# Kernel tuning notes

Measured on AMD Instinct MI355X. Metric: run time of the kernel, lower is better.

## Reference

```python
import jax, jax.numpy as jnp
import numpy as np

B, T, C, H = 4, 2048, 768, 12
D = C // H  # head dim = 64

def setup_inputs() -> dict:
    key = jax.random.key(0)
    k1, k2, k3 = jax.random.split(key, 3)
    x = jax.random.normal(k1, (B, T, C), dtype=jnp.float32)
    W_attn = jax.random.normal(k2, (C, 3 * C), dtype=jnp.float32) * 0.02
    b_attn = jnp.zeros((3 * C,), dtype=jnp.float32)
    W_proj = jax.random.normal(k3, (C, C), dtype=jnp.float32) * 0.02
    b_proj = jnp.zeros((C,), dtype=jnp.float32)
    return {"x": x, "W_attn": W_attn, "b_attn": b_attn, "W_proj": W_proj, "b_proj": b_proj}

def reference(x, W_attn, b_attn, W_proj, b_proj):
    Bx, Tx, Cx = x.shape
    qkv = x @ W_attn + b_attn                      # [B,T,3C]
    q, k, v = jnp.split(qkv, 3, axis=2)
    q = q.reshape(Bx, Tx, H, D).swapaxes(1, 2)     # [B,H,T,D]
    k = k.reshape(Bx, Tx, H, D).swapaxes(1, 2)
    v = v.reshape(Bx, Tx, H, D).swapaxes(1, 2)
    att = jnp.einsum('bhqd,bhkd->bhqk', q, k) / jnp.sqrt(jnp.float32(D))
    mask = jnp.tril(jnp.ones((Tx, Tx), dtype=bool))
    att = jnp.where(mask, att, -jnp.inf)
    att = jax.nn.softmax(att, axis=-1)
    y = jnp.einsum('bhqk,bhkd->bhqd', att, v)      # [B,H,T,D]
    y = y.swapaxes(1, 2).reshape(Bx, Tx, Cx)
    return y @ W_proj + b_proj
```

## Files before the change

kernel.cpp:

```cpp
#include <hip/hip_runtime.h>
#include <hip/hip_bf16.h>

#define BATCH 4
#define TSEQ  2048
#define CDIM  768
#define HNUM  12
#define DHEAD 64
#define NQKV  (3*CDIM)
#define BTOT  (BATCH*TSEQ)
#define BH    (BATCH*HNUM)

typedef unsigned short u16;
typedef __attribute__((ext_vector_type(8))) __bf16 bf16x8;
typedef __attribute__((ext_vector_type(4))) float f32x4;

#define MFMA16(a,b,c) __builtin_amdgcn_mfma_f32_16x16x32_bf16((a),(b),(c),0,0,0)

__device__ __forceinline__ u16 f2b(float f) {
    union { float f; unsigned u; } v; v.f = f;
    unsigned u = v.u;
    unsigned r = (u + 0x7fffu + ((u >> 16) & 1u)) >> 16;
    return (u16)r;
}

__device__ __forceinline__ unsigned cvtpk(float lo, float hi) {
    unsigned r;
    asm("v_cvt_pk_bf16_f32 %0, %1, %2" : "=v"(r) : "v"(lo), "v"(hi));
    return r;
}

__device__ __forceinline__ float fexp2(float x) {
    float r;
    asm("v_exp_f32 %0, %1" : "=v"(r) : "v"(x));
    return r;
}

__device__ __forceinline__ void gload_lds(const void* g, void* l) {
    __builtin_amdgcn_global_load_lds(
        (const __attribute__((address_space(1))) void*)g,
        (__attribute__((address_space(3))) void*)l, 16, 0, 0);
}

__global__ __launch_bounds__(256) void cast_f32_bf16(
        const float* __restrict__ in, u16* __restrict__ out, int n4) {
    int i = blockIdx.x * blockDim.x + threadIdx.x;
    if (i >= n4) return;
    float4 a = reinterpret_cast<const float4*>(in)[i];
    ushort4 o;
    o.x = f2b(a.x); o.y = f2b(a.y); o.z = f2b(a.z); o.w = f2b(a.w);
    reinterpret_cast<ushort4*>(out)[i] = o;
}

__global__ __launch_bounds__(256) void tcast(
        const float* __restrict__ in, u16* __restrict__ out, int R, int Cc) {
    __shared__ float tile[32][33];
    int c0 = blockIdx.x * 32, r0 = blockIdx.y * 32;
    int tx = threadIdx.x, ty = threadIdx.y;
    #pragma unroll
    for (int i = 0; i < 32; i += 8)
        tile[ty + i][tx] = in[(size_t)(r0 + ty + i) * Cc + c0 + tx];
    __syncthreads();
    #pragma unroll
    for (int i = 0; i < 32; i += 8)
        out[(size_t)(c0 + ty + i) * R + r0 + tx] = f2b(tile[tx][ty + i]);
}

template<int MODE>
__global__ __launch_bounds__(256) void gemm_bt(
        const u16* __restrict__ A, const u16* __restrict__ Bt,
        const float* __restrict__ bias,
        u16* __restrict__ qb, u16* __restrict__ kb, u16* __restrict__ vtb,
        float* __restrict__ outf, int M, int N, int K) {
    __shared__ u16 sA[2][128 * 32];
    __shared__ u16 sB[2][128 * 32];
    const int tid = threadIdx.x;
    const int lane = tid & 63;
    const int w = tid >> 6;
    const int wr = w >> 1, wc = w & 1;
    const int m0 = blockIdx.y * 128, n0 = blockIdx.x * 128;

    f32x4 acc[4][4] = {};

    auto stage = [&](int buf, int kt) {
        #pragma unroll
        for (int i = 0; i < 2; ++i) {
            int chunk = i * 256 + tid;
            int row = chunk >> 2, c8 = chunk & 3;
            gload_lds(A  + (size_t)(m0 + row) * K + kt * 32 + c8 * 8, &sA[buf][chunk * 8]);
            gload_lds(Bt + (size_t)(n0 + row) * K + kt * 32 + c8 * 8, &sB[buf][chunk * 8]);
        }
    };

    const int KT = K / 32;
    stage(0, 0);
    __syncthreads();
    for (int kt = 0; kt < KT; ++kt) {
        if (kt + 1 < KT) stage((kt + 1) & 1, kt + 1);
        const u16* cA = sA[kt & 1];
        const u16* cB = sB[kt & 1];
        bf16x8 af[4], bfr[4];
        #pragma unroll
        for (int m = 0; m < 4; ++m)
            af[m] = *(const bf16x8*)&cA[(wr * 64 + m * 16 + (lane & 15)) * 32 + ((lane >> 4) << 3)];
        #pragma unroll
        for (int n = 0; n < 4; ++n)
            bfr[n] = *(const bf16x8*)&cB[(wc * 64 + n * 16 + (lane & 15)) * 32 + ((lane >> 4) << 3)];
        #pragma unroll
        for (int m = 0; m < 4; ++m)
            #pragma unroll
            for (int n = 0; n < 4; ++n)
                acc[m][n] = MFMA16(af[m], bfr[n], acc[m][n]);
        __syncthreads();
    }

    if (MODE == 0) {
        const int which = n0 / CDIM;
        #pragma unroll
        for (int m = 0; m < 4; ++m) {
            #pragma unroll
            for (int n = 0; n < 4; ++n) {
                const int cg = n0 + wc * 64 + n * 16 + (lane & 15);
                const int c  = cg - which * CDIM;
                const int h  = c >> 6, d = c & 63;
                const float bv = bias[cg];
                const int rg0 = m0 + wr * 64 + m * 16 + ((lane >> 4) << 2);
                const int b = rg0 >> 11, t0 = rg0 & (TSEQ - 1);
                const size_t bh = (size_t)(b * HNUM + h);
                if (which == 2) {
                    ushort4 pv;
                    pv.x = f2b(acc[m][n][0] + bv);
                    pv.y = f2b(acc[m][n][1] + bv);
                    pv.z = f2b(acc[m][n][2] + bv);
                    pv.w = f2b(acc[m][n][3] + bv);
                    *(ushort4*)&vtb[(bh * DHEAD + d) * TSEQ + t0] = pv;
                } else {
                    #pragma unroll
                    for (int j = 0; j < 4; ++j) {
                        const float val = acc[m][n][j] + bv;
                        if (which == 0) qb[(bh * TSEQ + t0 + j) * DHEAD + d] = f2b(val * 0.1803368801111243f);
                        else            kb[(bh * TSEQ + t0 + j) * DHEAD + d] = f2b(val);
                    }
                }
            }
        }
    } else {
        #pragma unroll
        for (int m = 0; m < 4; ++m) {
            #pragma unroll
            for (int n = 0; n < 4; ++n) {
                const int cg = n0 + wc * 64 + n * 16 + (lane & 15);
                const float bv = bias[cg];
                #pragma unroll
                for (int j = 0; j < 4; ++j) {
                    const int rg = m0 + wr * 64 + m * 16 + ((lane >> 4) << 2) + j;
                    outf[(size_t)rg * CDIM + cg] = acc[m][n][j] + bv;
                }
            }
        }
    }
}

__global__ __launch_bounds__(256, 4) void attn_fwd(
        const u16* __restrict__ qb, const u16* __restrict__ kb,
        const u16* __restrict__ vtb, u16* __restrict__ yb) {
    __shared__ u16 sK[2][64 * 64];
    __shared__ u16 sVt[2][64 * 64];
    const int qt = 31 - (int)(blockIdx.x / BH);
    const int bh = blockIdx.x % BH;
    const int b = bh / HNUM, h = bh % HNUM;
    const int tid = threadIdx.x, lane = tid & 63, w = tid >> 6;
    const int g = lane >> 4, lq = lane & 15;
    const int qlo = qt * 64 + w * 16;
    const u16* qbase = qb  + (size_t)bh * TSEQ * DHEAD;
    const u16* kbase = kb  + (size_t)bh * TSEQ * DHEAD;
    const u16* vbase = vtb + (size_t)bh * DHEAD * TSEQ;

    bf16x8 qf[2];
    #pragma unroll
    for (int ks = 0; ks < 2; ++ks)
        qf[ks] = *(const bf16x8*)&qbase[(size_t)(qlo + lq) * DHEAD + ks * 32 + g * 8];

    union { unsigned u[4]; bf16x8 v; } ones;
    #pragma unroll
    for (int i = 0; i < 4; ++i) ones.u[i] = 0x3f803f80u;

    f32x4 o[4] = {};
    f32x4 ls = {};
    float mx = -__builtin_inff();

    auto STAGE = [&](int buf, int kt) {
        const int k0 = kt << 6;
        #pragma unroll
        for (int i = 0; i < 2; ++i) {
            int chunk = i * 256 + tid;
            int srow = chunk >> 3;
            int cb = ((chunk & 7) << 4) ^ ((srow & 7) << 4);
            gload_lds(kbase + (size_t)(k0 + srow) * DHEAD + (cb >> 1), &sK[buf][chunk * 8]);
            gload_lds(vbase + (size_t)srow * TSEQ + k0 + (cb >> 1),    &sVt[buf][chunk * 8]);
        }
    };

    const int nk = qt + 1;
    STAGE(0, 0);
    __syncthreads();
    for (int kt = 0; kt < nk; ++kt) {
        const int k0 = kt << 6;
        if (kt + 1 < nk) STAGE((kt + 1) & 1, kt + 1);
        const u16* cK = sK[kt & 1];
        const u16* cV = sVt[kt & 1];
        f32x4 s[4];
        #pragma unroll
        for (int n = 0; n < 4; ++n) s[n] = f32x4{0.f, 0.f, 0.f, 0.f};
        __builtin_amdgcn_s_setprio(1);
        #pragma unroll
        for (int n = 0; n < 4; ++n) {
            #pragma unroll
            for (int ks = 0; ks < 2; ++ks) {
                int r = n * 16 + lq;
                int lb = (r * 128 + (ks * 32 + g * 8) * 2) ^ ((r & 7) << 4);
                bf16x8 kf = *(const bf16x8*)((const char*)cK + lb);
                s[n] = MFMA16(kf, qf[ks], s[n]);
            }
        }
        __builtin_amdgcn_s_setprio(0);
        if (k0 + 63 > qlo) {
            const int qa = qlo + lq;
            #pragma unroll
            for (int n = 0; n < 4; ++n)
                #pragma unroll
                for (int j = 0; j < 4; ++j)
                    if (k0 + n * 16 + g * 4 + j > qa) s[n][j] = -__builtin_inff();
        }
        float t0 = fmaxf(fmaxf(s[0][0], s[0][1]), fmaxf(s[0][2], s[0][3]));
        float t1 = fmaxf(fmaxf(s[1][0], s[1][1]), fmaxf(s[1][2], s[1][3]));
        float t2 = fmaxf(fmaxf(s[2][0], s[2][1]), fmaxf(s[2][2], s[2][3]));
        float t3 = fmaxf(fmaxf(s[3][0], s[3][1]), fmaxf(s[3][2], s[3][3]));
        float tmax = fmaxf(fmaxf(t0, t1), fmaxf(t2, t3));
        tmax = fmaxf(tmax, __shfl_xor(tmax, 16));
        tmax = fmaxf(tmax, __shfl_xor(tmax, 32));
        if (__any(tmax > mx + 8.0f)) {
            float mnew = fmaxf(mx, tmax);
            float sc = fexp2(mx - mnew);
            mx = mnew;
            #pragma unroll
            for (int j = 0; j < 4; ++j) {
                float scj = __shfl(sc, (lane & 48) | ((g << 2) + j));
                ls[j] *= scj;
                #pragma unroll
                for (int n = 0; n < 4; ++n) o[n][j] *= scj;
            }
        }
        #pragma unroll
        for (int n = 0; n < 4; ++n)
            #pragma unroll
            for (int j = 0; j < 4; ++j)
                s[n][j] = fexp2(s[n][j] - mx);
        unsigned apk[4], bpk[4];
        #pragma unroll
        for (int n = 0; n < 4; ++n) {
            apk[n] = cvtpk(s[n][0], s[n][1]);
            bpk[n] = cvtpk(s[n][2], s[n][3]);
        }
        const int s0l = lq + ((lane & 16) << 1);
        const bool hi = (lane & 32) != 0;
        #pragma unroll
        for (int ks = 0; ks < 2; ++ks) {
            unsigned A0  = (unsigned)__shfl((int)apk[2 * ks],     s0l);
            unsigned B0  = (unsigned)__shfl((int)bpk[2 * ks],     s0l);
            unsigned A1  = (unsigned)__shfl((int)apk[2 * ks + 1], s0l);
            unsigned B1  = (unsigned)__shfl((int)bpk[2 * ks + 1], s0l);
            unsigned A0h = (unsigned)__shfl((int)apk[2 * ks],     s0l + 16);
            unsigned B0h = (unsigned)__shfl((int)bpk[2 * ks],     s0l + 16);
            unsigned A1h = (unsigned)__shfl((int)apk[2 * ks + 1], s0l + 16);
            unsigned B1h = (unsigned)__shfl((int)bpk[2 * ks + 1], s0l + 16);
            union { unsigned u[4]; bf16x8 v; } pa;
            pa.u[0] = hi ? A1  : A0;
            pa.u[1] = hi ? B1  : B0;
            pa.u[2] = hi ? A1h : A0h;
            pa.u[3] = hi ? B1h : B0h;
            __builtin_amdgcn_s_setprio(1);
            #pragma unroll
            for (int n = 0; n < 4; ++n) {
                int d = n * 16 + lq;
                int lb = (d * 128 + (ks * 32 + g * 8) * 2) ^ ((d & 7) << 4);
                bf16x8 vf = *(const bf16x8*)((const char*)cV + lb);
                o[n] = MFMA16(pa.v, vf, o[n]);
            }
            ls = MFMA16(pa.v, ones.v, ls);
            __builtin_amdgcn_s_setprio(0);
        }
        __syncthreads();
    }

    #pragma unroll
    for (int j = 0; j < 4; ++j) {
        float inv = 1.f / ls[j];
        const int t = qlo + g * 4 + j;
        #pragma unroll
        for (int n = 0; n < 4; ++n) {
            const int c = h * DHEAD + n * 16 + lq;
            yb[((size_t)b * TSEQ + t) * CDIM + c] = f2b(o[n][j] * inv);
        }
    }
}

extern "C" void kernel_launch(void* const* d_in, const int* in_sizes, int n_in,
                              void* d_out, int out_size, void* d_ws, size_t ws_size,
                              hipStream_t stream) {
    const float* x      = (const float*)d_in[0];
    const float* W_attn = (const float*)d_in[1];
    const float* b_attn = (const float*)d_in[2];
    const float* W_proj = (const float*)d_in[3];
    const float* b_proj = (const float*)d_in[4];
    float* out = (float*)d_out;

    u16* ws = (u16*)d_ws;
    u16* xb     = ws;
    u16* yb     = xb;
    u16* WattnT = xb     + (size_t)BTOT * CDIM;
    u16* WprojT = WattnT + (size_t)NQKV * CDIM;
    u16* qb     = WprojT + (size_t)CDIM * CDIM;
    u16* kb     = qb     + (size_t)BH * TSEQ * DHEAD;
    u16* vtb    = kb     + (size_t)BH * TSEQ * DHEAD;

    int n4 = BTOT * CDIM / 4;
    cast_f32_bf16<<<(n4 + 255) / 256, 256, 0, stream>>>(x, xb, n4);
    tcast<<<dim3(NQKV / 32, CDIM / 32), dim3(32, 8), 0, stream>>>(W_attn, WattnT, CDIM, NQKV);
    tcast<<<dim3(CDIM / 32, CDIM / 32), dim3(32, 8), 0, stream>>>(W_proj, WprojT, CDIM, CDIM);

    gemm_bt<0><<<dim3(NQKV / 128, BTOT / 128), 256, 0, stream>>>(
        xb, WattnT, b_attn, qb, kb, vtb, nullptr, BTOT, NQKV, CDIM);

    attn_fwd<<<dim3((TSEQ / 64) * BH), 256, 0, stream>>>(qb, kb, vtb, yb);

    gemm_bt<1><<<dim3(CDIM / 128, BTOT / 128), 256, 0, stream>>>(
        yb, WprojT, b_proj, nullptr, nullptr, nullptr, out, BTOT, CDIM, CDIM);
}
```

Baseline: 145.9 us.

## Swap MFMA operands for vectorized epilogue stores and remap GEMM blocks per XCD

Swaps the A/B operands of the MFMA so each lane holds four consecutive output columns instead of four consecutive rows. This lets the Q, K and projection-output epilogues use 4-wide vector stores and vector bias loads in place of scalar stores. V^T stores become scalar in exchange. It also flattens the GEMM grid to 1D and remaps block IDs so that consecutive tiles land on the same XCD (a blockIdx&7 swizzle), aiming to improve L2 reuse.

Measured after the change: 145.1 us. Within noise of the previous version (-0.6%).

```diff
diff --git a/kernel.cpp b/kernel.cpp
--- a/kernel.cpp
+++ b/kernel.cpp
@@ -65,7 +65,7 @@
         out[(size_t)(c0 + ty + i) * R + r0 + tx] = f2b(tile[tx][ty + i]);
 }
 
-template<int MODE>
+template<int MODE, int NX>
 __global__ __launch_bounds__(256) void gemm_bt(
         const u16* __restrict__ A, const u16* __restrict__ Bt,
         const float* __restrict__ bias,
@@ -77,7 +77,12 @@
     const int lane = tid & 63;
     const int w = tid >> 6;
     const int wr = w >> 1, wc = w & 1;
-    const int m0 = blockIdx.y * 128, n0 = blockIdx.x * 128;
+    const int nwg = NX * ((MODE == 0 ? BTOT : BTOT) / 128) ;
+    const int cpx = gridDim.x >> 3;
+    const int wg = ((int)blockIdx.x & 7) * cpx + ((int)blockIdx.x >> 3);
+    const int bx = wg % NX, by = wg / NX;
+    const int m0 = by * 128, n0 = bx * 128;
+    (void)nwg;
 
     f32x4 acc[4][4] = {};
 
@@ -109,7 +114,7 @@
         for (int m = 0; m < 4; ++m)
             #pragma unroll
             for (int n = 0; n < 4; ++n)
-                acc[m][n] = MFMA16(af[m], bfr[n], acc[m][n]);
+                acc[m][n] = MFMA16(bfr[n], af[m], acc[m][n]);
         __syncthreads();
     }
 
@@ -117,44 +122,51 @@
         const int which = n0 / CDIM;
         #pragma unroll
         for (int m = 0; m < 4; ++m) {
+            const int rg = m0 + wr * 64 + m * 16 + (lane & 15);
+            const int b = rg >> 11, t = rg & (TSEQ - 1);
             #pragma unroll
             for (int n = 0; n < 4; ++n) {
-                const int cg = n0 + wc * 64 + n * 16 + (lane & 15);
+                const int cg = n0 + wc * 64 + n * 16 + ((lane >> 4) << 2);
                 const int c  = cg - which * CDIM;
                 const int h  = c >> 6, d = c & 63;
-                const float bv = bias[cg];
-                const int rg0 = m0 + wr * 64 + m * 16 + ((lane >> 4) << 2);
-                const int b = rg0 >> 11, t0 = rg0 & (TSEQ - 1);
                 const size_t bh = (size_t)(b * HNUM + h);
-                if (which == 2) {
+                const float4 bv = *(const float4*)&bias[cg];
+                const float v0 = acc[m][n][0] + bv.x;
+                const float v1 = acc[m][n][1] + bv.y;
+                const float v2 = acc[m][n][2] + bv.z;
+                const float v3 = acc[m][n][3] + bv.w;
+                if (which == 0) {
+                    const float s = 0.1803368801111243f;
                     ushort4 pv;
-                    pv.x = f2b(acc[m][n][0] + bv);
-                    pv.y = f2b(acc[m][n][1] + bv);
-                    pv.z = f2b(acc[m][n][2] + bv);
-                    pv.w = f2b(acc[m][n][3] + bv);
-                    *(ushort4*)&vtb[(bh * DHEAD + d) * TSEQ + t0] = pv;
+                    pv.x = f2b(v0 * s); pv.y = f2b(v1 * s);
+                    pv.z = f2b(v2 * s); pv.w = f2b(v3 * s);
+                    *(ushort4*)&qb[(bh * TSEQ + t) * DHEAD + d] = pv;
+                } else if (which == 1) {
+                    ushort4 pv;
+                    pv.x = f2b(v0); pv.y = f2b(v1); pv.z = f2b(v2); pv.w = f2b(v3);
+                    *(ushort4*)&kb[(bh * TSEQ + t) * DHEAD + d] = pv;
                 } else {
-                    #pragma unroll
-                    for (int j = 0; j < 4; ++j) {
-                        const float val = acc[m][n][j] + bv;
-                        if (which == 0) qb[(bh * TSEQ + t0 + j) * DHEAD + d] = f2b(val * 0.1803368801111243f);
-                        else            kb[(bh * TSEQ + t0 + j) * DHEAD + d] = f2b(val);
-                    }
+                    vtb[(bh * DHEAD + d + 0) * TSEQ + t] = f2b(v0);
+                    vtb[(bh * DHEAD + d + 1) * TSEQ + t] = f2b(v1);
+                    vtb[(bh * DHEAD + d + 2) * TSEQ + t] = f2b(v2);
+                    vtb[(bh * DHEAD + d + 3) * TSEQ + t] = f2b(v3);
                 }
             }
         }
     } else {
         #pragma unroll
         for (int m = 0; m < 4; ++m) {
+            const int rg = m0 + wr * 64 + m * 16 + (lane & 15);
             #pragma unroll
             for (int n = 0; n < 4; ++n) {
-                const int cg = n0 + wc * 64 + n * 16 + (lane & 15);
-                const float bv = bias[cg];
-                #pragma unroll
-                for (int j = 0; j < 4; ++j) {
-                    const int rg = m0 + wr * 64 + m * 16 + ((lane >> 4) << 2) + j;
-                    outf[(size_t)rg * CDIM + cg] = acc[m][n][j] + bv;
-                }
+                const int cg = n0 + wc * 64 + n * 16 + ((lane >> 4) << 2);
+                const float4 bv = *(const float4*)&bias[cg];
+                float4 ov;
+                ov.x = acc[m][n][0] + bv.x;
+                ov.y = acc[m][n][1] + bv.y;
+                ov.z = acc[m][n][2] + bv.z;
+                ov.w = acc[m][n][3] + bv.w;
+                *(float4*)&outf[(size_t)rg * CDIM + cg] = ov;
             }
         }
     }
@@ -328,11 +340,11 @@
     tcast<<<dim3(NQKV / 32, CDIM / 32), dim3(32, 8), 0, stream>>>(W_attn, WattnT, CDIM, NQKV);
     tcast<<<dim3(CDIM / 32, CDIM / 32), dim3(32, 8), 0, stream>>>(W_proj, WprojT, CDIM, CDIM);
 
-    gemm_bt<0><<<dim3(NQKV / 128, BTOT / 128), 256, 0, stream>>>(
+    gemm_bt<0, NQKV / 128><<<dim3((NQKV / 128) * (BTOT / 128)), 256, 0, stream>>>(
         xb, WattnT, b_attn, qb, kb, vtb, nullptr, BTOT, NQKV, CDIM);
 
     attn_fwd<<<dim3((TSEQ / 64) * BH), 256, 0, stream>>>(qb, kb, vtb, yb);
 
-    gemm_bt<1><<<dim3(CDIM / 128, BTOT / 128), 256, 0, stream>>>(
+    gemm_bt<1, CDIM / 128><<<dim3((CDIM / 128) * (BTOT / 128)), 256, 0, stream>>>(
         yb, WprojT, b_proj, nullptr, nullptr, nullptr, out, BTOT, CDIM, CDIM);
 }
```
